# Optimization experiments

Hardware: AMD Instinct MI355X
Metric: run time of the kernel (lower is better)

Reference implementation:

```python
import jax, jax.numpy as jnp
import numpy as np
import math

T, E = 8192, 64            # tokens, experts
K_VALUE = 2                # top-2 router
CAP_FACTOR = 1.25          # capacity_factor_train (module in training mode)
MIN_CAPACITY = 4


def _get_capacity(tokens, experts):
    cap = math.floor(K_VALUE * CAP_FACTOR * tokens / experts)
    cap += cap % 2  # make even
    cap = max(cap, MIN_CAPACITY)
    assert cap > 0
    return int(cap)


def setup_inputs() -> dict:
    key = jax.random.key(0)
    inputs = jax.random.normal(key, (T, E), dtype=jnp.float32)
    return {"inputs": inputs}


def reference(inputs):
    tokens, experts = inputs.shape
    capacity = _get_capacity(tokens, experts)  # static (shape-derived)

    probs = jax.nn.softmax(inputs, axis=-1)                       # [T, E]
    top1_idx = jnp.argmax(probs, axis=-1)                         # [T]
    mask1 = jax.nn.one_hot(top1_idx, experts, dtype=jnp.int32)    # [T, E]
    probs_except1 = jnp.where(mask1.astype(bool), -jnp.inf, probs)
    top2_idx = jnp.argmax(probs_except1, axis=-1)                 # [T]
    mask2 = jax.nn.one_hot(top2_idx, experts, dtype=jnp.int32)

    # position of each token in its expert's queue (moe_cumsum = cumsum - 1)
    rank1 = jnp.cumsum(mask1, axis=0) - 1                          # [T, E]
    rank2 = jnp.cumsum(mask2, axis=0) - 1 + jnp.sum(mask1, axis=0, keepdims=True)

    # drop tokens beyond capacity
    mask1 = mask1 * (rank1 < capacity)
    mask2 = mask2 * (rank2 < capacity)
    used_capacity = mask1.sum(axis=0) + mask2.sum(axis=0)          # [E]

    # per-token slot index (0 if dropped) and gate weight (0 if dropped)
    r1 = jnp.sum(mask1 * rank1, axis=-1)                           # [T]
    r2 = jnp.sum(mask2 * rank2, axis=-1)
    w1 = jnp.sum(mask1 * probs, axis=-1)                           # [T]
    w2 = jnp.sum(mask2 * probs, axis=-1)
    m1b = jnp.sum(mask1, axis=-1).astype(bool)                     # kept flags
    m2b = jnp.sum(mask2, axis=-1).astype(bool)

    idx = jnp.arange(tokens)
    cb_weight = jnp.zeros((tokens, experts, capacity), dtype=inputs.dtype)
    cb_weight = cb_weight.at[idx, top1_idx, r1].add(w1)
    cb_weight = cb_weight.at[idx, top2_idx, r2].add(w2)

    sec_mask = jnp.zeros((tokens, experts, capacity), dtype=bool)
    sec_mask = sec_mask.at[idx, top1_idx, r1].max(m1b)
    sec_mask = sec_mask.at[idx, top2_idx, r2].max(m2b)

    return used_capacity, cb_weight, sec_mask
```

## Files before the change

kernel.cpp:

```cpp
#include <hip/hip_runtime.h>
#include <hip/hip_bf16.h>
#include <math.h>

#define T_TOKENS 8192
#define N_EXP    64
#define CAP      320
#define ROW4     (N_EXP * CAP / 4)

__global__ __launch_bounds__(256) void moe_topk_kernel(
    const float* __restrict__ in,
    int* __restrict__ top1, int* __restrict__ top2,
    float* __restrict__ w1, float* __restrict__ w2)
{
    const int token = blockIdx.x * 4 + (threadIdx.x >> 6);
    const int lane  = threadIdx.x & 63;
    if (token >= T_TOKENS) return;

    const float x = in[(size_t)token * N_EXP + lane];

    float v = x; int idx = lane;
    #pragma unroll
    for (int off = 32; off; off >>= 1) {
        float vo = __shfl_xor(v, off);
        int   io = __shfl_xor(idx, off);
        if (vo > v || (vo == v && io < idx)) { v = vo; idx = io; }
    }
    const float m  = v;
    const int   i1 = idx;

    float s = expf(x - m);
    #pragma unroll
    for (int off = 32; off; off >>= 1) s += __shfl_xor(s, off);

    float v2 = (lane == i1) ? -INFINITY : x;
    int idx2 = lane;
    #pragma unroll
    for (int off = 32; off; off >>= 1) {
        float vo = __shfl_xor(v2, off);
        int   io = __shfl_xor(idx2, off);
        if (vo > v2 || (vo == v2 && io < idx2)) { v2 = vo; idx2 = io; }
    }

    if (lane == 0) {
        top1[token] = i1;
        top2[token] = idx2;
        w1[token]   = 1.0f / s;
        w2[token]   = expf(v2 - m) / s;
    }
}

__global__ __launch_bounds__(256) void moe_rank_kernel(
    const int* __restrict__ top1, const int* __restrict__ top2,
    int* __restrict__ c1, int* __restrict__ c2,
    float* __restrict__ used)
{
    const int e    = blockIdx.x;
    const int tid  = threadIdx.x;
    const int lane = tid & 63;
    const int wid  = tid >> 6;

    __shared__ int wsum[4];

    const unsigned long long below_mask = (lane == 63)
        ? 0x7FFFFFFFFFFFFFFFull
        : ((1ull << lane) - 1ull);

    int base = 0;
    for (int t0 = 0; t0 < T_TOKENS; t0 += 256) {
        const int  t     = t0 + tid;
        const bool match = (top1[t] == e);
        const unsigned long long mb = __ballot(match);
        const int below = __popcll(mb & below_mask);
        if (lane == 0) wsum[wid] = __popcll(mb);
        __syncthreads();
        int pre = 0;
        for (int w = 0; w < wid; ++w) pre += wsum[w];
        const int tot = wsum[0] + wsum[1] + wsum[2] + wsum[3];
        if (match) {
            const int r = base + pre + below;
            c1[t] = (r < CAP) ? (e * CAP + r) : -1;
        }
        base += tot;
        __syncthreads();
    }
    const int count1 = base;

    int base2 = 0;
    for (int t0 = 0; t0 < T_TOKENS; t0 += 256) {
        const int  t     = t0 + tid;
        const bool match = (top2[t] == e);
        const unsigned long long mb = __ballot(match);
        const int below = __popcll(mb & below_mask);
        if (lane == 0) wsum[wid] = __popcll(mb);
        __syncthreads();
        int pre = 0;
        for (int w = 0; w < wid; ++w) pre += wsum[w];
        const int tot = wsum[0] + wsum[1] + wsum[2] + wsum[3];
        if (match) {
            const int r = count1 + base2 + pre + below;
            c2[t] = (r < CAP) ? (e * CAP + r) : -1;
        }
        base2 += tot;
        __syncthreads();
    }
    const int count2 = base2;

    if (tid == 0) {
        const int kept1 = min(count1, CAP);
        const int kept2 = min(max(CAP - count1, 0), count2);
        used[e] = (float)(kept1 + kept2);
    }
}

__global__ __launch_bounds__(256) void moe_row_write_kernel(
    const int* __restrict__ c1, const int* __restrict__ c2,
    const float* __restrict__ w1, const float* __restrict__ w2,
    float* __restrict__ out)
{
    const int t   = blockIdx.x;
    const int tid = threadIdx.x;

    const int   p1 = c1[t];
    const int   p2 = c2[t];
    const float a  = w1[t];
    const float b  = w2[t];
    const int   q1 = p1 >> 2;
    const int   q2 = p2 >> 2;

    float4* __restrict__ cb  = (float4*)(out + N_EXP) + (size_t)t * ROW4;
    float4* __restrict__ sec = cb + (size_t)T_TOKENS * ROW4;

    #pragma unroll
    for (int i = 0; i < ROW4 / 256; ++i) {
        const int idx  = i * 256 + tid;
        const int base = idx * 4;
        float4 v = make_float4(0.f, 0.f, 0.f, 0.f);
        float4 s = make_float4(0.f, 0.f, 0.f, 0.f);
        if (idx == q1 || idx == q2) {
            float* vp = (float*)&v;
            float* sp = (float*)&s;
            #pragma unroll
            for (int j = 0; j < 4; ++j) {
                const int pos = base + j;
                float vv = 0.f, ss = 0.f;
                if (pos == p1) { vv += a; ss = 1.f; }
                if (pos == p2) { vv += b; ss = 1.f; }
                vp[j] = vv; sp[j] = ss;
            }
        }
        cb[idx]  = v;
        sec[idx] = s;
    }
}

extern "C" void kernel_launch(void* const* d_in, const int* in_sizes, int n_in,
                              void* d_out, int out_size, void* d_ws, size_t ws_size,
                              hipStream_t stream) {
    const float* in  = (const float*)d_in[0];
    float*       out = (float*)d_out;

    int*   top1 = (int*)d_ws;
    int*   top2 = top1 + T_TOKENS;
    int*   c1   = top2 + T_TOKENS;
    int*   c2   = c1 + T_TOKENS;
    float* w1   = (float*)(c2 + T_TOKENS);
    float* w2   = w1 + T_TOKENS;

    moe_topk_kernel<<<T_TOKENS / 4, 256, 0, stream>>>(in, top1, top2, w1, w2);
    moe_rank_kernel<<<N_EXP, 256, 0, stream>>>(top1, top2, c1, c2, out);
    moe_row_write_kernel<<<T_TOKENS, 256, 0, stream>>>(c1, c2, w1, w2, out + 0);
}
```

Before: 287.4 us.

## Rewrite rank kernel as single-pass block scan and use nontemporal output stores

```diff
diff --git a/kernel.cpp b/kernel.cpp
--- a/kernel.cpp
+++ b/kernel.cpp
@@ -6,6 +6,8 @@
 #define N_EXP    64
 #define CAP      320
 #define ROW4     (N_EXP * CAP / 4)
+
+typedef float f32x4 __attribute__((ext_vector_type(4)));
 
 __global__ __launch_bounds__(256) void moe_topk_kernel(
     const float* __restrict__ in,
@@ -49,7 +51,7 @@
     }
 }
 
-__global__ __launch_bounds__(256) void moe_rank_kernel(
+__global__ __launch_bounds__(1024) void moe_rank_kernel(
     const int* __restrict__ top1, const int* __restrict__ top2,
     int* __restrict__ c1, int* __restrict__ c2,
     float* __restrict__ used)
@@ -59,55 +61,79 @@
     const int lane = tid & 63;
     const int wid  = tid >> 6;
 
-    __shared__ int wsum[4];
+    __shared__ int wsA[16], wsB[16];
 
-    const unsigned long long below_mask = (lane == 63)
-        ? 0x7FFFFFFFFFFFFFFFull
-        : ((1ull << lane) - 1ull);
+    const int4 a1 = ((const int4*)top1)[tid * 2];
+    const int4 b1 = ((const int4*)top1)[tid * 2 + 1];
+    const int m0 = (a1.x == e), m1 = (a1.y == e), m2 = (a1.z == e), m3 = (a1.w == e);
+    const int m4 = (b1.x == e), m5 = (b1.y == e), m6 = (b1.z == e), m7 = (b1.w == e);
+    const int cnt1 = m0 + m1 + m2 + m3 + m4 + m5 + m6 + m7;
 
-    int base = 0;
-    for (int t0 = 0; t0 < T_TOKENS; t0 += 256) {
-        const int  t     = t0 + tid;
-        const bool match = (top1[t] == e);
-        const unsigned long long mb = __ballot(match);
-        const int below = __popcll(mb & below_mask);
-        if (lane == 0) wsum[wid] = __popcll(mb);
-        __syncthreads();
-        int pre = 0;
-        for (int w = 0; w < wid; ++w) pre += wsum[w];
-        const int tot = wsum[0] + wsum[1] + wsum[2] + wsum[3];
-        if (match) {
-            const int r = base + pre + below;
-            c1[t] = (r < CAP) ? (e * CAP + r) : -1;
-        }
-        base += tot;
-        __syncthreads();
+    int sc = cnt1;
+    #pragma unroll
+    for (int off = 1; off < 64; off <<= 1) {
+        int n = __shfl_up(sc, off);
+        if (lane >= off) sc += n;
     }
-    const int count1 = base;
+    if (lane == 63) wsA[wid] = sc;
+    __syncthreads();
+    int wbase = 0, total1 = 0;
+    #pragma unroll
+    for (int w = 0; w < 16; ++w) {
+        const int sv = wsA[w];
+        if (w < wid) wbase += sv;
+        total1 += sv;
+    }
+    {
+        int r = wbase + sc - cnt1;
+        const int t0 = tid * 8;
+        if (m0) { c1[t0 + 0] = (r < CAP) ? (e * CAP + r) : -1; ++r; }
+        if (m1) { c1[t0 + 1] = (r < CAP) ? (e * CAP + r) : -1; ++r; }
+        if (m2) { c1[t0 + 2] = (r < CAP) ? (e * CAP + r) : -1; ++r; }
+        if (m3) { c1[t0 + 3] = (r < CAP) ? (e * CAP + r) : -1; ++r; }
+        if (m4) { c1[t0 + 4] = (r < CAP) ? (e * CAP + r) : -1; ++r; }
+        if (m5) { c1[t0 + 5] = (r < CAP) ? (e * CAP + r) : -1; ++r; }
+        if (m6) { c1[t0 + 6] = (r < CAP) ? (e * CAP + r) : -1; ++r; }
+        if (m7) { c1[t0 + 7] = (r < CAP) ? (e * CAP + r) : -1; ++r; }
+    }
 
-    int base2 = 0;
-    for (int t0 = 0; t0 < T_TOKENS; t0 += 256) {
-        const int  t     = t0 + tid;
-        const bool match = (top2[t] == e);
-        const unsigned long long mb = __ballot(match);
-        const int below = __popcll(mb & below_mask);
-        if (lane == 0) wsum[wid] = __popcll(mb);
-        __syncthreads();
-        int pre = 0;
-        for (int w = 0; w < wid; ++w) pre += wsum[w];
-        const int tot = wsum[0] + wsum[1] + wsum[2] + wsum[3];
-        if (match) {
-            const int r = count1 + base2 + pre + below;
-            c2[t] = (r < CAP) ? (e * CAP + r) : -1;
-        }
-        base2 += tot;
-        __syncthreads();
+    const int4 a2 = ((const int4*)top2)[tid * 2];
+    const int4 b2 = ((const int4*)top2)[tid * 2 + 1];
+    const int n0 = (a2.x == e), n1 = (a2.y == e), n2 = (a2.z == e), n3 = (a2.w == e);
+    const int n4 = (b2.x == e), n5 = (b2.y == e), n6 = (b2.z == e), n7 = (b2.w == e);
+    const int cnt2 = n0 + n1 + n2 + n3 + n4 + n5 + n6 + n7;
+
+    int sc2 = cnt2;
+    #pragma unroll
+    for (int off = 1; off < 64; off <<= 1) {
+        int n = __shfl_up(sc2, off);
+        if (lane >= off) sc2 += n;
     }
-    const int count2 = base2;
+    if (lane == 63) wsB[wid] = sc2;
+    __syncthreads();
+    int wbase2 = 0, total2 = 0;
+    #pragma unroll
+    for (int w = 0; w < 16; ++w) {
+        const int sv = wsB[w];
+        if (w < wid) wbase2 += sv;
+        total2 += sv;
+    }
+    {
+        int r = total1 + wbase2 + sc2 - cnt2;
+        const int t0 = tid * 8;
+        if (n0) { c2[t0 + 0] = (r < CAP) ? (e * CAP + r) : -1; ++r; }
+        if (n1) { c2[t0 + 1] = (r < CAP) ? (e * CAP + r) : -1; ++r; }
+        if (n2) { c2[t0 + 2] = (r < CAP) ? (e * CAP + r) : -1; ++r; }
+        if (n3) { c2[t0 + 3] = (r < CAP) ? (e * CAP + r) : -1; ++r; }
+        if (n4) { c2[t0 + 4] = (r < CAP) ? (e * CAP + r) : -1; ++r; }
+        if (n5) { c2[t0 + 5] = (r < CAP) ? (e * CAP + r) : -1; ++r; }
+        if (n6) { c2[t0 + 6] = (r < CAP) ? (e * CAP + r) : -1; ++r; }
+        if (n7) { c2[t0 + 7] = (r < CAP) ? (e * CAP + r) : -1; ++r; }
+    }
 
     if (tid == 0) {
-        const int kept1 = min(count1, CAP);
-        const int kept2 = min(max(CAP - count1, 0), count2);
+        const int kept1 = min(total1, CAP);
+        const int kept2 = min(max(CAP - total1, 0), total2);
         used[e] = (float)(kept1 + kept2);
     }
 }
@@ -127,29 +153,27 @@
     const int   q1 = p1 >> 2;
     const int   q2 = p2 >> 2;
 
-    float4* __restrict__ cb  = (float4*)(out + N_EXP) + (size_t)t * ROW4;
-    float4* __restrict__ sec = cb + (size_t)T_TOKENS * ROW4;
+    f32x4* __restrict__ cb  = (f32x4*)(out + N_EXP) + (size_t)t * ROW4;
+    f32x4* __restrict__ sec = cb + (size_t)T_TOKENS * ROW4;
 
     #pragma unroll
     for (int i = 0; i < ROW4 / 256; ++i) {
-        const int idx  = i * 256 + tid;
-        const int base = idx * 4;
-        float4 v = make_float4(0.f, 0.f, 0.f, 0.f);
-        float4 s = make_float4(0.f, 0.f, 0.f, 0.f);
+        const int idx = i * 256 + tid;
+        f32x4 v = {0.f, 0.f, 0.f, 0.f};
+        f32x4 s = {0.f, 0.f, 0.f, 0.f};
         if (idx == q1 || idx == q2) {
-            float* vp = (float*)&v;
-            float* sp = (float*)&s;
+            const int base = idx * 4;
             #pragma unroll
             for (int j = 0; j < 4; ++j) {
                 const int pos = base + j;
                 float vv = 0.f, ss = 0.f;
                 if (pos == p1) { vv += a; ss = 1.f; }
                 if (pos == p2) { vv += b; ss = 1.f; }
-                vp[j] = vv; sp[j] = ss;
+                v[j] = vv; s[j] = ss;
             }
         }
-        cb[idx]  = v;
-        sec[idx] = s;
+        __builtin_nontemporal_store(v, cb + idx);
+        __builtin_nontemporal_store(s, sec + idx);
     }
 }
 
@@ -167,6 +191,6 @@
     float* w2   = w1 + T_TOKENS;
 
     moe_topk_kernel<<<T_TOKENS / 4, 256, 0, stream>>>(in, top1, top2, w1, w2);
-    moe_rank_kernel<<<N_EXP, 256, 0, stream>>>(top1, top2, c1, c2, out);
-    moe_row_write_kernel<<<T_TOKENS, 256, 0, stream>>>(c1, c2, w1, w2, out + 0);
+    moe_rank_kernel<<<N_EXP, 1024, 0, stream>>>(top1, top2, c1, c2, out);
+    moe_row_write_kernel<<<T_TOKENS, 256, 0, stream>>>(c1, c2, w1, w2, out);
 }
```

Result: faster. 270.1 us (-6.0%).
